# Kernel tuning notes

Measured on AMD Instinct MI355X. Metric: run time of the kernel, lower is better.

## Reference

```python
import jax, jax.numpy as jnp
import numpy as np

B, H, N, D = 16, 8, 256, 32


def setup_inputs() -> dict:
    key = jax.random.key(0)
    k1, k2, k3 = jax.random.split(key, 3)
    q = jax.random.normal(k1, (B, H, N, D), dtype=jnp.float32)
    k = jax.random.normal(k2, (B, H, N, D), dtype=jnp.float32)
    scale = jnp.ones((1,), dtype=jnp.float32)  # unused by the module
    mask = jnp.zeros((B, 1, N, N), dtype=bool)  # True == masked out
    # learned attention vector, xavier_uniform over (1, H, 1, 1, D)
    fan = 1 * H * 1 * 1 * D
    bound = float(np.sqrt(6.0 / (1 + D)))  # xavier for (..., D) param
    attention = jax.random.uniform(k3, (1, H, 1, 1, D), dtype=jnp.float32,
                                   minval=-bound, maxval=bound)
    return {"q": q, "k": k, "scale": scale, "mask": mask, "attention": attention}


def reference(q, k, scale, mask, attention):
    # summed: [B, H, Nq, Nk, D] via broadcast of q.unsqueeze(-2)+k.unsqueeze(-3)
    summed = q[:, :, :, None, :] + k[:, :, None, :, :]
    # GATv2 score: a^T * silu(q_i + k_j), reduced over head_dim
    scores = jnp.sum(jax.nn.silu(summed) * attention, axis=-1)  # [B, H, Nq, Nk]
    neg = jnp.finfo(scores.dtype).min
    scores_masked = jnp.where(mask, neg, scores)
    attn = jax.nn.softmax(scores_masked, axis=-1)
    return attn
```

## Files before the change

kernel.cpp:

```cpp
#include <hip/hip_runtime.h>
#include <stdint.h>
#include <stddef.h>

constexpr int Bc = 16, Hc = 8, Nc = 256, Dc = 32;
constexpr float LOG2E = 1.44269504088896340736f;

constexpr int    MF    = 10;
constexpr double PHALF = 9.7;
constexpr double LFIT  = 9.0;

constexpr double PI_ = 3.14159265358979323846;

constexpr double cexp_(double x) {
    int n = (int)(x >= 0 ? x + 0.5 : x - 0.5);
    double f = x - n, t = 1.0, s = 1.0;
    for (int i = 1; i <= 26; ++i) { t *= f / i; s += t; }
    const double E = 2.71828182845904523536;
    double en = 1.0, bb = n >= 0 ? E : 1.0 / E;
    int an = n < 0 ? -n : n;
    for (int i = 0; i < an; ++i) en *= bb;
    return s * en;
}
constexpr double creduce_(double x) {
    while (x >  PI_) x -= 2.0 * PI_;
    while (x < -PI_) x += 2.0 * PI_;
    return x;
}
constexpr double ccos_(double x0) {
    double x = creduce_(x0), x2 = x * x, t = 1.0, s = 1.0;
    for (int i = 1; i <= 16; ++i) { t *= -x2 / ((2.0*i - 1.0) * (2.0*i)); s += t; }
    return s;
}
constexpr double csin_(double x0) {
    double x = creduce_(x0), x2 = x * x, t = x, s = x;
    for (int i = 1; i <= 16; ++i) { t *= -x2 / ((2.0*i) * (2.0*i + 1.0)); s += t; }
    return s;
}
constexpr double Gfun_(double x) {
    double z = x < 0 ? -x : x;
    double e = cexp_(z);
    return 0.5 * z * ((e - 1.0) / (e + 1.0));
}
constexpr double csqrt_(double x) {
    if (x <= 0) return 0;
    double r = x > 1 ? x : 1;
    for (int i = 0; i < 40; ++i) r = 0.5 * (r + x / r);
    return r;
}

struct FitT { float tk[MF + 1]; float tq[MF + 1]; };

constexpr FitT lsFit_() {
    constexpr int NB = MF + 1;
    double A[NB][NB] = {}, bv[NB] = {};
    for (int p = 0; p < NB; ++p)
        for (int qq = 0; qq < NB; ++qq) {
            double wm = (p - qq) * PI_ / PHALF, wp = (p + qq) * PI_ / PHALF;
            double Sm = (p == qq)     ? LFIT : csin_(wm * LFIT) / wm;
            double Sp = (p + qq == 0) ? LFIT : csin_(wp * LFIT) / wp;
            A[p][qq] = 0.5 * (Sm + Sp);
        }
    constexpr int NS = 128;
    double hh = LFIT / NS, gx[NS + 1] = {};
    for (int i = 0; i <= NS; ++i) gx[i] = Gfun_(i * hh);
    for (int p = 0; p < NB; ++p) {
        double s = 0;
        for (int i = 0; i <= NS; ++i) {
            double wgt = (i == 0 || i == NS) ? 1.0 : ((i & 1) ? 4.0 : 2.0);
            s += wgt * gx[i] * ccos_(p * PI_ / PHALF * (i * hh));
        }
        bv[p] = s * hh / 3.0;
    }
    for (int p = 0; p < NB; ++p) A[p][p] += 1e-8 * LFIT;
    for (int col = 0; col < NB; ++col) {
        int piv = col; double best = A[col][col] < 0 ? -A[col][col] : A[col][col];
        for (int r = col + 1; r < NB; ++r) {
            double v = A[r][col] < 0 ? -A[r][col] : A[r][col];
            if (v > best) { best = v; piv = r; }
        }
        if (piv != col) {
            for (int cc = 0; cc < NB; ++cc) { double t = A[col][cc]; A[col][cc] = A[piv][cc]; A[piv][cc] = t; }
            double t = bv[col]; bv[col] = bv[piv]; bv[piv] = t;
        }
        for (int r = col + 1; r < NB; ++r) {
            double f = A[r][col] / A[col][col];
            for (int cc = col; cc < NB; ++cc) A[r][cc] -= f * A[col][cc];
            bv[r] -= f * bv[col];
        }
    }
    double c[NB] = {};
    for (int r = NB - 1; r >= 0; --r) {
        double s = bv[r];
        for (int cc = r + 1; cc < NB; ++cc) s -= A[r][cc] * c[cc];
        c[r] = s / A[r][r];
    }
    FitT f{};
    for (int m = 0; m <= MF; ++m) {
        double rt = csqrt_(c[m] < 0 ? -c[m] : c[m]);
        f.tk[m] = (float)rt;
        f.tq[m] = (float)(c[m] < 0 ? -rt : rt);
    }
    return f;
}
constexpr FitT CF = lsFit_();

typedef _Float16 half8  __attribute__((ext_vector_type(8)));
typedef float    f32x16 __attribute__((ext_vector_type(16)));

__device__ __forceinline__ uint32_t pkh_(float a, float b) {
    auto v = __builtin_amdgcn_cvt_pkrtz(a, b);
    uint32_t u; __builtin_memcpy(&u, &v, 4); return u;
}

constexpr int KB_  = Nc * 128;
constexpr int QB_  = 128 * 128;
constexpr int BUF  = KB_ + QB_;
constexpr int SRED_OFF = 2 * BUF;
constexpr int AKV_OFF  = SRED_OFF + 2048;
constexpr int SMEM     = AKV_OFF + 1024;

__global__ __launch_bounds__(1024, 4) void gatv2_mfma_kernel(
    const float* __restrict__ q, const float* __restrict__ k,
    const uint8_t* __restrict__ mask, const float* __restrict__ att,
    float* __restrict__ out)
{
    extern __shared__ char smem[];
    float* sred = (float*)(smem + SRED_OFF);
    float* akv  = (float*)(smem + AKV_OFF);

    const int tid = threadIdx.x, lane = tid & 63, w = tid >> 6;
    const int bh = blockIdx.y, h = bh & 7, b = bh >> 3;
    const int iBlk = blockIdx.x * 128;
    const float invTwoP = (float)(1.0 / (2.0 * PHALF));

    const int dq = tid & 7, rw = tid >> 3;
    const float4 a4 = *(const float4*)(att + h * Dc + 4 * dq);
    const int swS = (dq ^ (rw & 7)) << 4;

    const float* kbase = k + (size_t)bh * Nc * Dc;
    float kc1[8], ks1[8], kcm[8], ksm[8];
    int offK[2];
#pragma unroll
    for (int it = 0; it < 2; ++it) {
        const int j = rw + it * 128;
        const float4 kv = *(const float4*)(kbase + j * Dc + 4 * dq);
        float part = a4.x * kv.x + a4.y * kv.y + a4.z * kv.z + a4.w * kv.w;
        part += __shfl_xor(part, 1, 64);
        part += __shfl_xor(part, 2, 64);
        part += __shfl_xor(part, 4, 64);
        if (dq == 0) akv[j] = part;
        const float rv[4] = { kv.x, kv.y, kv.z, kv.w };
#pragma unroll
        for (int c = 0; c < 4; ++c) {
            float r = __builtin_amdgcn_fractf(rv[c] * invTwoP);
            kc1[4*it+c] = __builtin_amdgcn_cosf(r);
            ks1[4*it+c] = __builtin_amdgcn_sinf(r);
            kcm[4*it+c] = kc1[4*it+c];
            ksm[4*it+c] = ks1[4*it+c];
        }
        offK[it] = j * 128 + swS;
    }
    const float* qbase = q + ((size_t)bh * Nc + iBlk) * Dc;
    float qc1[4], qs1[4], qcm[4], qsm[4];
    const int offQ = KB_ + rw * 128 + swS;
    {
        const float4 qv = *(const float4*)(qbase + rw * Dc + 4 * dq);
        const float rv[4] = { qv.x, qv.y, qv.z, qv.w };
#pragma unroll
        for (int c = 0; c < 4; ++c) {
            float r = __builtin_amdgcn_fractf(rv[c] * invTwoP);
            qc1[c] = __builtin_amdgcn_cosf(r);
            qs1[c] = __builtin_amdgcn_sinf(r);
            qcm[c] = qc1[c]; qsm[c] = qs1[c];
        }
    }

    const int hi5 = lane >> 5, col = lane & 31;
    const int wi = w & 3, wj = w >> 2;
    const int baseA  = KB_ + (wi * 32 + col) * 128;
    const int baseB0 = (wj * 64 + col) * 128, baseB1 = baseB0 + 32 * 128;
    const int sA = col & 7;

    f32x16 acc[2];
#pragma unroll
    for (int jt = 0; jt < 2; ++jt)
#pragma unroll
        for (int e = 0; e < 16; ++e) acc[jt][e] = 0.0f;

    auto buildWrite = [&](int mN, int dstOff) {
        const float tk = CF.tk[mN];
        const float g0 = CF.tq[mN]*a4.x, g1 = CF.tq[mN]*a4.y;
        const float g2 = CF.tq[mN]*a4.z, g3 = CF.tq[mN]*a4.w;
#pragma unroll
        for (int it = 0; it < 2; ++it) {
            uint4 wv;
            wv.x = pkh_(tk * kcm[4*it+0], tk * ksm[4*it+0]);
            wv.y = pkh_(tk * kcm[4*it+1], tk * ksm[4*it+1]);
            wv.z = pkh_(tk * kcm[4*it+2], tk * ksm[4*it+2]);
            wv.w = pkh_(tk * kcm[4*it+3], tk * ksm[4*it+3]);
            *(uint4*)(smem + dstOff + offK[it]) = wv;
        }
        {
            uint4 wv;
            wv.x = pkh_(g0 * qcm[0], -(g0 * qsm[0]));
            wv.y = pkh_(g1 * qcm[1], -(g1 * qsm[1]));
            wv.z = pkh_(g2 * qcm[2], -(g2 * qsm[2]));
            wv.w = pkh_(g3 * qcm[3], -(g3 * qsm[3]));
            *(uint4*)(smem + dstOff + offQ) = wv;
        }
    };
    auto rotate = [&]() {
#pragma unroll
        for (int e = 0; e < 8; ++e) {
            float cn = fmaf(kc1[e], kcm[e], -(ks1[e] * ksm[e]));
            float sn = fmaf(ks1[e], kcm[e],   kc1[e] * ksm[e]);
            kcm[e] = cn; ksm[e] = sn;
        }
#pragma unroll
        for (int e = 0; e < 4; ++e) {
            float cn = fmaf(qc1[e], qcm[e], -(qs1[e] * qsm[e]));
            float sn = fmaf(qs1[e], qcm[e],   qc1[e] * qsm[e]);
            qcm[e] = cn; qsm[e] = sn;
        }
    };
    auto loadFrags = [&](int srcOff, int s, half8& A, half8& B0, half8& B1) {
        const int du = ((2 * s + hi5) ^ sA) << 4;
        A  = *(const half8*)(smem + srcOff + baseA  + du);
        B0 = *(const half8*)(smem + srcOff + baseB0 + du);
        B1 = *(const half8*)(smem + srcOff + baseB1 + du);
    };

    buildWrite(1, 0);
    rotate();
    __syncthreads();
#pragma unroll
    for (int m = 1; m <= MF; ++m) {
        const int srcOff = ((m - 1) & 1) * BUF;
        const int dstOff = (m & 1) * BUF;
        half8 A0, B00, B10, A1, B01, B11;
        loadFrags(srcOff, 0, A0, B00, B10);
        loadFrags(srcOff, 1, A1, B01, B11);
        if (m < MF) { buildWrite(m + 1, dstOff); rotate(); }
        __builtin_amdgcn_s_setprio(1);
        acc[0] = __builtin_amdgcn_mfma_f32_32x32x16_f16(A0, B00, acc[0], 0, 0, 0);
        acc[1] = __builtin_amdgcn_mfma_f32_32x32x16_f16(A0, B10, acc[1], 0, 0, 0);
        loadFrags(srcOff, 2, A0, B00, B10);
        acc[0] = __builtin_amdgcn_mfma_f32_32x32x16_f16(A1, B01, acc[0], 0, 0, 0);
        acc[1] = __builtin_amdgcn_mfma_f32_32x32x16_f16(A1, B11, acc[1], 0, 0, 0);
        loadFrags(srcOff, 3, A1, B01, B11);
        acc[0] = __builtin_amdgcn_mfma_f32_32x32x16_f16(A0, B00, acc[0], 0, 0, 0);
        acc[1] = __builtin_amdgcn_mfma_f32_32x32x16_f16(A0, B10, acc[1], 0, 0, 0);
        acc[0] = __builtin_amdgcn_mfma_f32_32x32x16_f16(A1, B01, acc[0], 0, 0, 0);
        acc[1] = __builtin_amdgcn_mfma_f32_32x32x16_f16(A1, B11, acc[1], 0, 0, 0);
        __builtin_amdgcn_s_setprio(0);
        if (m < MF) __syncthreads();
    }

    constexpr float M0 = 24.0f;
    const int jB = wj * 64;
    const float akj0 = akv[jB + col], akj1 = akv[jB + 32 + col];
    const int iB = iBlk + wi * 32;

    float v[16];
#pragma unroll
    for (int e = 0; e < 16; ++e) {
        const int rloc = (e & 3) + 8 * (e >> 2) + 4 * hi5;
        const int ig = iB + rloc;
        const uint8_t* mr = mask + ((size_t)(b * Nc + ig)) * Nc + jB + col;
        float v0 = fmaf(0.5f, akj0, acc[0][e]);
        float v1 = fmaf(0.5f, akj1, acc[1][e]);
        if (mr[0])  v0 = -1.0e30f;
        if (mr[32]) v1 = -1.0e30f;
        float p0 = __builtin_amdgcn_exp2f(__builtin_fminf((v0 - M0) * LOG2E, 80.0f));
        float p1 = __builtin_amdgcn_exp2f(__builtin_fminf((v1 - M0) * LOG2E, 80.0f));
        acc[0][e] = p0;
        acc[1][e] = p1;
        v[e] = p0 + p1;
    }
    float u8[8];
#pragma unroll
    for (int j = 0; j < 8; ++j) {
        float mine = (col & 16) ? v[j + 8] : v[j];
        float send = (col & 16) ? v[j]     : v[j + 8];
        u8[j] = mine + __shfl_xor(send, 16, 64);
    }
    float u4[4];
#pragma unroll
    for (int j = 0; j < 4; ++j) {
        float mine = (col & 8) ? u8[j + 4] : u8[j];
        float send = (col & 8) ? u8[j]     : u8[j + 4];
        u4[j] = mine + __shfl_xor(send, 8, 64);
    }
    float u2[2];
#pragma unroll
    for (int j = 0; j < 2; ++j) {
        float mine = (col & 4) ? u4[j + 2] : u4[j];
        float send = (col & 4) ? u4[j]     : u4[j + 2];
        u2[j] = mine + __shfl_xor(send, 4, 64);
    }
    float t1;
    {
        float mine = (col & 2) ? u2[1] : u2[0];
        float send = (col & 2) ? u2[0] : u2[1];
        t1 = mine + __shfl_xor(send, 2, 64);
    }
    t1 += __shfl_xor(t1, 1, 64);
    {
        const int eL = ((col & 16) ? 8 : 0) + ((col & 8) ? 4 : 0)
                     + ((col & 4) ? 2 : 0) + ((col & 2) ? 1 : 0);
        const int rl = (eL & 3) + 8 * (eL >> 2) + 4 * hi5;
        if (!(col & 1)) sred[(wi * 32 + rl) * 4 + wj] = t1;
    }
    __syncthreads();

    float* obase = out + (size_t)bh * Nc * Nc;
#pragma unroll
    for (int e = 0; e < 16; ++e) {
        const int rloc = (e & 3) + 8 * (e >> 2) + 4 * hi5;
        const int iL = wi * 32 + rloc;
        const int ig = iB + rloc;
        const float4 tv = *(const float4*)(&sred[iL * 4]);
        const float inv = __builtin_amdgcn_rcpf(tv.x + tv.y + tv.z + tv.w);
        obase[(size_t)ig * Nc + jB + col]      = acc[0][e] * inv;
        obase[(size_t)ig * Nc + jB + 32 + col] = acc[1][e] * inv;
    }
}

extern "C" void kernel_launch(void* const* d_in, const int* in_sizes, int n_in,
                              void* d_out, int out_size, void* d_ws, size_t ws_size,
                              hipStream_t stream) {
    const float*   q    = (const float*)d_in[0];
    const float*   k    = (const float*)d_in[1];
    const uint8_t* mask = (const uint8_t*)d_in[3];
    const float*   att  = (const float*)d_in[4];
    float*         out  = (float*)d_out;

    (void)hipFuncSetAttribute((const void*)gatv2_mfma_kernel,
                              hipFuncAttributeMaxDynamicSharedMemorySize, SMEM);

    dim3 grid(2, Bc * Hc);
    dim3 block(1024);
    gatv2_mfma_kernel<<<grid, block, SMEM, stream>>>(q, k, mask, att, out);
}
```

Before: 97.09 us.

## Halve block size and give each wave a 64x64 register tile

```diff
diff --git a/kernel.cpp b/kernel.cpp
--- a/kernel.cpp
+++ b/kernel.cpp
@@ -119,7 +119,7 @@
 constexpr int AKV_OFF  = SRED_OFF + 2048;
 constexpr int SMEM     = AKV_OFF + 1024;
 
-__global__ __launch_bounds__(1024, 4) void gatv2_mfma_kernel(
+__global__ __launch_bounds__(512, 2) void gatv2_mfma_kernel(
     const float* __restrict__ q, const float* __restrict__ k,
     const uint8_t* __restrict__ mask, const float* __restrict__ att,
     float* __restrict__ out)
@@ -138,11 +138,11 @@
     const int swS = (dq ^ (rw & 7)) << 4;
 
     const float* kbase = k + (size_t)bh * Nc * Dc;
-    float kc1[8], ks1[8], kcm[8], ksm[8];
-    int offK[2];
-#pragma unroll
-    for (int it = 0; it < 2; ++it) {
-        const int j = rw + it * 128;
+    float kc1[16], ks1[16], kcm[16], ksm[16];
+    int offK[4];
+#pragma unroll
+    for (int it = 0; it < 4; ++it) {
+        const int j = rw + it * 64;
         const float4 kv = *(const float4*)(kbase + j * Dc + 4 * dq);
         float part = a4.x * kv.x + a4.y * kv.y + a4.z * kv.z + a4.w * kv.w;
         part += __shfl_xor(part, 1, 64);
@@ -161,38 +161,44 @@
         offK[it] = j * 128 + swS;
     }
     const float* qbase = q + ((size_t)bh * Nc + iBlk) * Dc;
-    float qc1[4], qs1[4], qcm[4], qsm[4];
-    const int offQ = KB_ + rw * 128 + swS;
-    {
-        const float4 qv = *(const float4*)(qbase + rw * Dc + 4 * dq);
+    float qc1[8], qs1[8], qcm[8], qsm[8];
+    int offQ[2];
+#pragma unroll
+    for (int it = 0; it < 2; ++it) {
+        const int iq = rw + it * 64;
+        const float4 qv = *(const float4*)(qbase + iq * Dc + 4 * dq);
         const float rv[4] = { qv.x, qv.y, qv.z, qv.w };
 #pragma unroll
         for (int c = 0; c < 4; ++c) {
             float r = __builtin_amdgcn_fractf(rv[c] * invTwoP);
-            qc1[c] = __builtin_amdgcn_cosf(r);
-            qs1[c] = __builtin_amdgcn_sinf(r);
-            qcm[c] = qc1[c]; qsm[c] = qs1[c];
-        }
+            qc1[4*it+c] = __builtin_amdgcn_cosf(r);
+            qs1[4*it+c] = __builtin_amdgcn_sinf(r);
+            qcm[4*it+c] = qc1[4*it+c];
+            qsm[4*it+c] = qs1[4*it+c];
+        }
+        offQ[it] = KB_ + iq * 128 + swS;
     }
 
     const int hi5 = lane >> 5, col = lane & 31;
-    const int wi = w & 3, wj = w >> 2;
-    const int baseA  = KB_ + (wi * 32 + col) * 128;
-    const int baseB0 = (wj * 64 + col) * 128, baseB1 = baseB0 + 32 * 128;
+    const int wi = w & 1, wj = w >> 1;
+    const int baseA0 = KB_ + (wi * 64 + col) * 128, baseA1 = baseA0 + 32 * 128;
+    const int baseB0 = (wj * 64 + col) * 128,       baseB1 = baseB0 + 32 * 128;
     const int sA = col & 7;
 
-    f32x16 acc[2];
-#pragma unroll
-    for (int jt = 0; jt < 2; ++jt)
-#pragma unroll
-        for (int e = 0; e < 16; ++e) acc[jt][e] = 0.0f;
+    f32x16 acc[2][2];
+#pragma unroll
+    for (int i2 = 0; i2 < 2; ++i2)
+#pragma unroll
+        for (int j2 = 0; j2 < 2; ++j2)
+#pragma unroll
+            for (int e = 0; e < 16; ++e) acc[i2][j2][e] = 0.0f;
 
     auto buildWrite = [&](int mN, int dstOff) {
         const float tk = CF.tk[mN];
         const float g0 = CF.tq[mN]*a4.x, g1 = CF.tq[mN]*a4.y;
         const float g2 = CF.tq[mN]*a4.z, g3 = CF.tq[mN]*a4.w;
 #pragma unroll
-        for (int it = 0; it < 2; ++it) {
+        for (int it = 0; it < 4; ++it) {
             uint4 wv;
             wv.x = pkh_(tk * kcm[4*it+0], tk * ksm[4*it+0]);
             wv.y = pkh_(tk * kcm[4*it+1], tk * ksm[4*it+1]);
@@ -200,35 +206,44 @@
             wv.w = pkh_(tk * kcm[4*it+3], tk * ksm[4*it+3]);
             *(uint4*)(smem + dstOff + offK[it]) = wv;
         }
-        {
+#pragma unroll
+        for (int it = 0; it < 2; ++it) {
             uint4 wv;
-            wv.x = pkh_(g0 * qcm[0], -(g0 * qsm[0]));
-            wv.y = pkh_(g1 * qcm[1], -(g1 * qsm[1]));
-            wv.z = pkh_(g2 * qcm[2], -(g2 * qsm[2]));
-            wv.w = pkh_(g3 * qcm[3], -(g3 * qsm[3]));
-            *(uint4*)(smem + dstOff + offQ) = wv;
+            wv.x = pkh_(g0 * qcm[4*it+0], -(g0 * qsm[4*it+0]));
+            wv.y = pkh_(g1 * qcm[4*it+1], -(g1 * qsm[4*it+1]));
+            wv.z = pkh_(g2 * qcm[4*it+2], -(g2 * qsm[4*it+2]));
+            wv.w = pkh_(g3 * qcm[4*it+3], -(g3 * qsm[4*it+3]));
+            *(uint4*)(smem + dstOff + offQ[it]) = wv;
         }
     };
     auto rotate = [&]() {
 #pragma unroll
-        for (int e = 0; e < 8; ++e) {
+        for (int e = 0; e < 16; ++e) {
             float cn = fmaf(kc1[e], kcm[e], -(ks1[e] * ksm[e]));
             float sn = fmaf(ks1[e], kcm[e],   kc1[e] * ksm[e]);
             kcm[e] = cn; ksm[e] = sn;
         }
 #pragma unroll
-        for (int e = 0; e < 4; ++e) {
+        for (int e = 0; e < 8; ++e) {
             float cn = fmaf(qc1[e], qcm[e], -(qs1[e] * qsm[e]));
             float sn = fmaf(qs1[e], qcm[e],   qc1[e] * qsm[e]);
             qcm[e] = cn; qsm[e] = sn;
         }
     };
-    auto loadFrags = [&](int srcOff, int s, half8& A, half8& B0, half8& B1) {
+    auto loadFrags = [&](int srcOff, int s, half8& A0, half8& A1,
+                         half8& B0, half8& B1) {
         const int du = ((2 * s + hi5) ^ sA) << 4;
-        A  = *(const half8*)(smem + srcOff + baseA  + du);
+        A0 = *(const half8*)(smem + srcOff + baseA0 + du);
+        A1 = *(const half8*)(smem + srcOff + baseA1 + du);
         B0 = *(const half8*)(smem + srcOff + baseB0 + du);
         B1 = *(const half8*)(smem + srcOff + baseB1 + du);
     };
+    auto mfma4 = [&](half8 A0, half8 A1, half8 B0, half8 B1) {
+        acc[0][0] = __builtin_amdgcn_mfma_f32_32x32x16_f16(A0, B0, acc[0][0], 0, 0, 0);
+        acc[0][1] = __builtin_amdgcn_mfma_f32_32x32x16_f16(A0, B1, acc[0][1], 0, 0, 0);
+        acc[1][0] = __builtin_amdgcn_mfma_f32_32x32x16_f16(A1, B0, acc[1][0], 0, 0, 0);
+        acc[1][1] = __builtin_amdgcn_mfma_f32_32x32x16_f16(A1, B1, acc[1][1], 0, 0, 0);
+    };
 
     buildWrite(1, 0);
     rotate();
@@ -237,21 +252,17 @@
     for (int m = 1; m <= MF; ++m) {
         const int srcOff = ((m - 1) & 1) * BUF;
         const int dstOff = (m & 1) * BUF;
-        half8 A0, B00, B10, A1, B01, B11;
-        loadFrags(srcOff, 0, A0, B00, B10);
-        loadFrags(srcOff, 1, A1, B01, B11);
+        half8 A0a, A1a, B0a, B1a, A0b, A1b, B0b, B1b;
+        loadFrags(srcOff, 0, A0a, A1a, B0a, B1a);
+        loadFrags(srcOff, 1, A0b, A1b, B0b, B1b);
         if (m < MF) { buildWrite(m + 1, dstOff); rotate(); }
         __builtin_amdgcn_s_setprio(1);
-        acc[0] = __builtin_amdgcn_mfma_f32_32x32x16_f16(A0, B00, acc[0], 0, 0, 0);
-        acc[1] = __builtin_amdgcn_mfma_f32_32x32x16_f16(A0, B10, acc[1], 0, 0, 0);
-        loadFrags(srcOff, 2, A0, B00, B10);
-        acc[0] = __builtin_amdgcn_mfma_f32_32x32x16_f16(A1, B01, acc[0], 0, 0, 0);
-        acc[1] = __builtin_amdgcn_mfma_f32_32x32x16_f16(A1, B11, acc[1], 0, 0, 0);
-        loadFrags(srcOff, 3, A1, B01, B11);
-        acc[0] = __builtin_amdgcn_mfma_f32_32x32x16_f16(A0, B00, acc[0], 0, 0, 0);
-        acc[1] = __builtin_amdgcn_mfma_f32_32x32x16_f16(A0, B10, acc[1], 0, 0, 0);
-        acc[0] = __builtin_amdgcn_mfma_f32_32x32x16_f16(A1, B01, acc[0], 0, 0, 0);
-        acc[1] = __builtin_amdgcn_mfma_f32_32x32x16_f16(A1, B11, acc[1], 0, 0, 0);
+        mfma4(A0a, A1a, B0a, B1a);
+        loadFrags(srcOff, 2, A0a, A1a, B0a, B1a);
+        mfma4(A0b, A1b, B0b, B1b);
+        loadFrags(srcOff, 3, A0b, A1b, B0b, B1b);
+        mfma4(A0a, A1a, B0a, B1a);
+        mfma4(A0b, A1b, B0b, B1b);
         __builtin_amdgcn_s_setprio(0);
         if (m < MF) __syncthreads();
     }
@@ -259,70 +270,77 @@
     constexpr float M0 = 24.0f;
     const int jB = wj * 64;
     const float akj0 = akv[jB + col], akj1 = akv[jB + 32 + col];
-    const int iB = iBlk + wi * 32;
-
-    float v[16];
+    const int iB = iBlk + wi * 64;
+
+#pragma unroll
+    for (int i2 = 0; i2 < 2; ++i2) {
+        float v[16];
+#pragma unroll
+        for (int e = 0; e < 16; ++e) {
+            const int rloc = (e & 3) + 8 * (e >> 2) + 4 * hi5;
+            const int ig = iB + i2 * 32 + rloc;
+            const uint8_t* mr = mask + ((size_t)(b * Nc + ig)) * Nc + jB + col;
+            float v0 = fmaf(0.5f, akj0, acc[i2][0][e]);
+            float v1 = fmaf(0.5f, akj1, acc[i2][1][e]);
+            if (mr[0])  v0 = -1.0e30f;
+            if (mr[32]) v1 = -1.0e30f;
+            float p0 = __builtin_amdgcn_exp2f(__builtin_fminf((v0 - M0) * LOG2E, 80.0f));
+            float p1 = __builtin_amdgcn_exp2f(__builtin_fminf((v1 - M0) * LOG2E, 80.0f));
+            acc[i2][0][e] = p0;
+            acc[i2][1][e] = p1;
+            v[e] = p0 + p1;
+        }
+        float u8[8];
+#pragma unroll
+        for (int jj = 0; jj < 8; ++jj) {
+            float mine = (col & 16) ? v[jj + 8] : v[jj];
+            float send = (col & 16) ? v[jj]     : v[jj + 8];
+            u8[jj] = mine + __shfl_xor(send, 16, 64);
+        }
+        float u4[4];
+#pragma unroll
+        for (int jj = 0; jj < 4; ++jj) {
+            float mine = (col & 8) ? u8[jj + 4] : u8[jj];
+            float send = (col & 8) ? u8[jj]     : u8[jj + 4];
+            u4[jj] = mine + __shfl_xor(send, 8, 64);
+        }
+        float u2[2];
+#pragma unroll
+        for (int jj = 0; jj < 2; ++jj) {
+            float mine = (col & 4) ? u2[0] * 0.0f + ((col & 4) ? u4[jj + 2] : u4[jj]) : u4[jj];
+            (void)mine;
+            float mn = (col & 4) ? u4[jj + 2] : u4[jj];
+            float sd = (col & 4) ? u4[jj]     : u4[jj + 2];
+            u2[jj] = mn + __shfl_xor(sd, 4, 64);
+        }
+        float t1;
+        {
+            float mn = (col & 2) ? u2[1] : u2[0];
+            float sd = (col & 2) ? u2[0] : u2[1];
+            t1 = mn + __shfl_xor(sd, 2, 64);
+        }
+        t1 += __shfl_xor(t1, 1, 64);
+        {
+            const int eL = ((col & 16) ? 8 : 0) + ((col & 8) ? 4 : 0)
+                         + ((col & 4) ? 2 : 0) + ((col & 2) ? 1 : 0);
+            const int rl = (eL & 3) + 8 * (eL >> 2) + 4 * hi5;
+            if (!(col & 1)) sred[(wi * 64 + i2 * 32 + rl) * 4 + wj] = t1;
+        }
+    }
+    __syncthreads();
+
+    float* obase = out + (size_t)bh * Nc * Nc;
+#pragma unroll
+    for (int i2 = 0; i2 < 2; ++i2)
 #pragma unroll
     for (int e = 0; e < 16; ++e) {
         const int rloc = (e & 3) + 8 * (e >> 2) + 4 * hi5;
-        const int ig = iB + rloc;
-        const uint8_t* mr = mask + ((size_t)(b * Nc + ig)) * Nc + jB + col;
-        float v0 = fmaf(0.5f, akj0, acc[0][e]);
-        float v1 = fmaf(0.5f, akj1, acc[1][e]);
-        if (mr[0])  v0 = -1.0e30f;
-        if (mr[32]) v1 = -1.0e30f;
-        float p0 = __builtin_amdgcn_exp2f(__builtin_fminf((v0 - M0) * LOG2E, 80.0f));
-        float p1 = __builtin_amdgcn_exp2f(__builtin_fminf((v1 - M0) * LOG2E, 80.0f));
-        acc[0][e] = p0;
-        acc[1][e] = p1;
-        v[e] = p0 + p1;
-    }
-    float u8[8];
-#pragma unroll
-    for (int j = 0; j < 8; ++j) {
-        float mine = (col & 16) ? v[j + 8] : v[j];
-        float send = (col & 16) ? v[j]     : v[j + 8];
-        u8[j] = mine + __shfl_xor(send, 16, 64);
-    }
-    float u4[4];
-#pragma unroll
-    for (int j = 0; j < 4; ++j) {
-        float mine = (col & 8) ? u8[j + 4] : u8[j];
-        float send = (col & 8) ? u8[j]     : u8[j + 4];
-        u4[j] = mine + __shfl_xor(send, 8, 64);
-    }
-    float u2[2];
-#pragma unroll
-    for (int j = 0; j < 2; ++j) {
-        float mine = (col & 4) ? u4[j + 2] : u4[j];
-        float send = (col & 4) ? u4[j]     : u4[j + 2];
-        u2[j] = mine + __shfl_xor(send, 4, 64);
-    }
-    float t1;
-    {
-        float mine = (col & 2) ? u2[1] : u2[0];
-        float send = (col & 2) ? u2[0] : u2[1];
-        t1 = mine + __shfl_xor(send, 2, 64);
-    }
-    t1 += __shfl_xor(t1, 1, 64);
-    {
-        const int eL = ((col & 16) ? 8 : 0) + ((col & 8) ? 4 : 0)
-                     + ((col & 4) ? 2 : 0) + ((col & 2) ? 1 : 0);
-        const int rl = (eL & 3) + 8 * (eL >> 2) + 4 * hi5;
-        if (!(col & 1)) sred[(wi * 32 + rl) * 4 + wj] = t1;
-    }
-    __syncthreads();
-
-    float* obase = out + (size_t)bh * Nc * Nc;
-#pragma unroll
-    for (int e = 0; e < 16; ++e) {
-        const int rloc = (e & 3) + 8 * (e >> 2) + 4 * hi5;
-        const int iL = wi * 32 + rloc;
-        const int ig = iB + rloc;
+        const int iL = wi * 64 + i2 * 32 + rloc;
+        const int ig = iBlk + iL;
         const float4 tv = *(const float4*)(&sred[iL * 4]);
         const float inv = __builtin_amdgcn_rcpf(tv.x + tv.y + tv.z + tv.w);
-        obase[(size_t)ig * Nc + jB + col]      = acc[0][e] * inv;
-        obase[(size_t)ig * Nc + jB + 32 + col] = acc[1][e] * inv;
+        obase[(size_t)ig * Nc + jB + col]      = acc[i2][0][e] * inv;
+        obase[(size_t)ig * Nc + jB + 32 + col] = acc[i2][1][e] * inv;
     }
 }
 
@@ -339,6 +357,6 @@
                               hipFuncAttributeMaxDynamicSharedMemorySize, SMEM);
 
     dim3 grid(2, Bc * Hc);
-    dim3 block(1024);
+    dim3 block(512);
     gatv2_mfma_kernel<<<grid, block, SMEM, stream>>>(q, k, mask, att, out);
 }
```

Measured after the change: 92.22 us. 5.0% less time.
